# Kernel optimization log

Hardware: AMD Instinct MI355X
Metric: run time of the kernel (lower is better)

## Reference

```python
import jax, jax.numpy as jnp
import numpy as np

B, T, D = 32, 512, 256
F = 256  # duration_predictor_filter_size
K = 3    # kernel size, padding=1
MEL_MAX = 2304
EPS = 1e-5


def _conv1d(x, w, b):
    # x: [B, T, C_in], w: [C_out, C_in, K], 'same'-ish padding=1
    y = jax.lax.conv_general_dilated(
        x.transpose(0, 2, 1), w, window_strides=(1,), padding=[(1, 1)],
        dimension_numbers=("NCH", "OIH", "NCH"))
    return y.transpose(0, 2, 1) + b


def _layernorm(x, g, b):
    mu = jnp.mean(x, axis=-1, keepdims=True)
    var = jnp.mean(jnp.square(x - mu), axis=-1, keepdims=True)
    return (x - mu) * jax.lax.rsqrt(var + EPS) * g + b


def setup_inputs() -> dict:
    key = jax.random.key(0)
    ks = jax.random.split(key, 8)
    x = jax.random.normal(ks[0], (B, T, D), dtype=jnp.float32)
    target = jax.random.randint(ks[1], (B, T), 0, 8, dtype=jnp.int32)
    s = 0.02
    return {
        "x": x,
        "target": target,
        "mel_max_length": MEL_MAX,
        "conv1_w": jax.random.normal(ks[2], (F, D, K), dtype=jnp.float32) * s,
        "conv1_b": jnp.zeros((F,), jnp.float32),
        "ln1_g": jnp.ones((F,), jnp.float32),
        "ln1_b": jnp.zeros((F,), jnp.float32),
        "conv2_w": jax.random.normal(ks[3], (F, F, K), dtype=jnp.float32) * s,
        "conv2_b": jnp.zeros((F,), jnp.float32),
        "ln2_g": jnp.ones((F,), jnp.float32),
        "ln2_b": jnp.zeros((F,), jnp.float32),
        "lin_w": jax.random.normal(ks[4], (1, F), dtype=jnp.float32) * s,
        "lin_b": jnp.zeros((1,), jnp.float32),
    }


def reference(x, target, mel_max_length, conv1_w, conv1_b, ln1_g, ln1_b,
              conv2_w, conv2_b, ln2_g, ln2_b, lin_w, lin_b):
    # Variance_adaptor (duration predictor), eval-mode dropout = identity
    h = jax.nn.relu(_layernorm(_conv1d(x, conv1_w, conv1_b), ln1_g, ln1_b))
    h = jax.nn.relu(_layernorm(_conv1d(h, conv2_w, conv2_b), ln2_g, ln2_b))
    dur_pred = jax.nn.relu(jnp.einsum("btf,of->bto", h, lin_w) + lin_b)[..., 0]  # [B,T]

    # LR: alignment @ x, expressed as the equivalent duration-indexed gather.
    # alignment[b, t_out, j] = 1 iff cumsum(dur)[b,j-1] <= t_out < cumsum(dur)[b,j]
    cum = jnp.cumsum(target, axis=1)                    # [B, T]
    t_out = jnp.arange(mel_max_length, dtype=cum.dtype)  # [T_out]
    idx = jax.vmap(lambda c: jnp.searchsorted(c, t_out, side="right"))(cum)  # [B, T_out]
    valid = (t_out[None, :] < cum[:, -1:]).astype(x.dtype)                   # [B, T_out]
    gathered = jnp.take_along_axis(x, jnp.clip(idx, 0, T - 1)[:, :, None], axis=1)
    output = gathered * valid[:, :, None]                # zeros past total length (pad)
    return output, dur_pred
```

## Files before the change

kernel.cpp:

```cpp
#include <hip/hip_runtime.h>

typedef __attribute__((ext_vector_type(8))) short short8;
typedef __attribute__((ext_vector_type(4))) float floatx4;

typedef __attribute__((address_space(3))) unsigned int lds_u32;
typedef __attribute__((address_space(1))) const unsigned int glb_u32;

static __device__ __forceinline__ unsigned short f2bf(float f) {
    unsigned int u = __float_as_uint(f);
    return (unsigned short)((u + 0x7FFFu + ((u >> 16) & 1u)) >> 16);
}
static __device__ __forceinline__ void cp16(const ushort* g, ushort* l) {
    __builtin_amdgcn_global_load_lds((glb_u32*)g, (lds_u32*)l, 16, 0, 0);
}

__global__ __launch_bounds__(256)
void prep_kernel(const float* __restrict__ x, const float* __restrict__ w1,
                 const float* __restrict__ w2,
                 ushort* __restrict__ xb, ushort* __restrict__ h1b,
                 ushort* __restrict__ w1pb, ushort* __restrict__ w2pb)
{
    const int blk = blockIdx.x, tid = threadIdx.x;
    if (blk < 4112) {
        const int r = blk * 4 + (tid >> 6);
        const int c = (tid & 63) * 4;
        const int b = r / 514, tp = r % 514;
        ushort4 o;
        if (tp >= 1 && tp <= 512) {
            float4 v = *(const float4*)(x + ((size_t)(b * 512 + tp - 1) * 256 + c));
            o.x = f2bf(v.x); o.y = f2bf(v.y); o.z = f2bf(v.z); o.w = f2bf(v.w);
        } else {
            o.x = o.y = o.z = o.w = 0;
            *(ushort4*)(h1b + (size_t)r * 256 + c) = o;
        }
        *(ushort4*)(xb + (size_t)r * 256 + c) = o;
    } else {
        const bool second = blk >= 4880;
        const int e = (blk - (second ? 4880 : 4112)) * 256 + tid;
        const float* w = second ? w2 : w1;
        ushort* wpb = second ? w2pb : w1pb;
        const int f = e / 768, j = e % 768;
        const int c = j & 255, kr = j >> 8;
        const int s = j >> 6, kk = j & 63;
        wpb[s * 16384 + f * 64 + (((kk >> 3) ^ (f & 7)) << 3) + (kk & 7)]
            = f2bf(w[f * 768 + c * 3 + kr]);
    }
}

template<bool IS_CONV2>
__global__ __launch_bounds__(256, 2)
void conv_mfma_kernel(const ushort* __restrict__ xb,
                      const ushort* __restrict__ wpb,
                      const float* __restrict__ cbias,
                      const float* __restrict__ gamma, const float* __restrict__ beta,
                      const float* __restrict__ lw, const float* __restrict__ lb,
                      ushort* __restrict__ outb,
                      float* __restrict__ durp,
                      const float* __restrict__ x,
                      const int* __restrict__ target,
                      float* __restrict__ out0)
{
    __shared__ ushort As[32 * 64];
    __shared__ ushort Bs[256 * 64];
    __shared__ float sum_s[4][32], sq_s[4][32], mu_s[32], rs_s[32];
    __shared__ int cum[512], ps[256], sidx[64];

    const int tid = threadIdx.x;

    if (IS_CONV2 && blockIdx.x >= 512) {
        const int bg = blockIdx.x - 512;
        const int b = bg / 36, t0o = (bg % 36) * 64;
        const int v0 = target[b * 512 + 2 * tid];
        const int v1 = target[b * 512 + 2 * tid + 1];
        ps[tid] = v0 + v1;
        __syncthreads();
        for (int off = 1; off < 256; off <<= 1) {
            int t = (tid >= off) ? ps[tid - off] : 0;
            __syncthreads();
            ps[tid] += t;
            __syncthreads();
        }
        const int excl = tid ? ps[tid - 1] : 0;
        cum[2 * tid]     = excl + v0;
        cum[2 * tid + 1] = excl + v0 + v1;
        __syncthreads();
        const int total = cum[511];
        if (tid < 64) {
            int t = t0o + tid;
            int lo = 0, hi = 512;
            while (lo < hi) {
                int mid = (lo + hi) >> 1;
                if (cum[mid] <= t) lo = mid + 1; else hi = mid;
            }
            sidx[tid] = (t < total) ? ((lo < 512) ? lo : 511) : -1;
        }
        __syncthreads();
        const float4* x4 = (const float4*)x;
        float4* o4 = (float4*)out0;
        const int lane6 = tid & 63, g4 = tid >> 6;
        #pragma unroll 4
        for (int rr = 0; rr < 16; ++rr) {
            int r = rr * 4 + g4;
            int idx = sidx[r];
            float4 v = make_float4(0.f, 0.f, 0.f, 0.f);
            if (idx >= 0) v = x4[((size_t)(b * 512 + idx)) * 64 + lane6];
            o4[((size_t)(b * 2304 + t0o + r)) * 64 + lane6] = v;
        }
        return;
    }

    const int w_ = tid >> 6, lane = tid & 63;
    const int q = lane >> 4, col = lane & 15;
    const int b  = blockIdx.x & 31;
    const int t0 = (blockIdx.x >> 5) << 5;
    const int rot = blockIdx.x % 12;

    floatx4 acc[2][4] = {};
    const ushort* xbb = xb + (size_t)b * 514 * 256;
    const int arow = tid >> 3, aquad = (tid & 7) ^ (arow & 7);
    ushort* AsW = As + (size_t)w_ * 512;
    ushort* BsW = Bs + (size_t)w_ * 512;

    for (int s = 0; s < 12; ++s) {
        int se = s + rot; if (se >= 12) se -= 12;
        const int krow = se >> 2, cbo = (se & 3) << 6;
        cp16(xbb + (size_t)(t0 + krow + arow) * 256 + cbo + aquad * 8, AsW);
        const ushort* wsrc = wpb + (size_t)se * 16384 + w_ * 512 + lane * 8;
        #pragma unroll
        for (int i = 0; i < 8; ++i) cp16(wsrc + i * 2048, BsW + i * 2048);
        __syncthreads();
        short8 af[2][2], bf[4][2];
        #pragma unroll
        for (int mi = 0; mi < 2; ++mi)
            #pragma unroll
            for (int kh = 0; kh < 2; ++kh)
                af[mi][kh] = *(const short8*)((const char*)As
                    + (mi * 16 + col) * 128 + (((kh * 4 + q) ^ (col & 7)) * 16));
        #pragma unroll
        for (int ni = 0; ni < 4; ++ni)
            #pragma unroll
            for (int kh = 0; kh < 2; ++kh)
                bf[ni][kh] = *(const short8*)((const char*)Bs
                    + (w_ * 64 + ni * 16 + col) * 128 + (((kh * 4 + q) ^ (col & 7)) * 16));
        #pragma unroll
        for (int kh = 0; kh < 2; ++kh)
            #pragma unroll
            for (int mi = 0; mi < 2; ++mi)
                #pragma unroll
                for (int ni = 0; ni < 4; ++ni)
                    acc[mi][ni] = __builtin_amdgcn_mfma_f32_16x16x32_bf16(
                        af[mi][kh], bf[ni][kh], acc[mi][ni], 0, 0, 0);
        __syncthreads();
    }

    const int base_c = w_ * 64;
    float cb4[4], gm4[4], bt4[4];
    #pragma unroll
    for (int ni = 0; ni < 4; ++ni) {
        cb4[ni] = cbias[base_c + ni * 16 + col];
        gm4[ni] = gamma[base_c + ni * 16 + col];
        bt4[ni] = beta [base_c + ni * 16 + col];
    }
    float rsum[2][4] = {}, rsq[2][4] = {};
    #pragma unroll
    for (int mi = 0; mi < 2; ++mi)
        #pragma unroll
        for (int ni = 0; ni < 4; ++ni)
            #pragma unroll
            for (int r = 0; r < 4; ++r) {
                float v = acc[mi][ni][r] + cb4[ni];
                acc[mi][ni][r] = v;
                rsum[mi][r] += v;
                rsq [mi][r] += v * v;
            }
    #pragma unroll
    for (int mi = 0; mi < 2; ++mi)
        #pragma unroll
        for (int r = 0; r < 4; ++r) {
            float s = rsum[mi][r], ss = rsq[mi][r];
            #pragma unroll
            for (int d = 8; d > 0; d >>= 1) {
                s  += __shfl_down(s,  d, 16);
                ss += __shfl_down(ss, d, 16);
            }
            if (col == 0) {
                sum_s[w_][mi * 16 + q * 4 + r] = s;
                sq_s [w_][mi * 16 + q * 4 + r] = ss;
            }
        }
    __syncthreads();
    if (tid < 32) {
        float s  = sum_s[0][tid] + sum_s[1][tid] + sum_s[2][tid] + sum_s[3][tid];
        float ss = sq_s [0][tid] + sq_s [1][tid] + sq_s [2][tid] + sq_s [3][tid];
        float mu = s * (1.f / 256.f);
        mu_s[tid] = mu;
        rs_s[tid] = rsqrtf(ss * (1.f / 256.f) - mu * mu + 1e-5f);
    }
    __syncthreads();

    if (!IS_CONV2) {
        #pragma unroll
        for (int mi = 0; mi < 2; ++mi)
            #pragma unroll
            for (int ni = 0; ni < 4; ++ni)
                #pragma unroll
                for (int r = 0; r < 4; ++r) {
                    int row = mi * 16 + q * 4 + r;
                    float v = (acc[mi][ni][r] - mu_s[row]) * rs_s[row] * gm4[ni] + bt4[ni];
                    outb[((size_t)b * 514 + t0 + row + 1) * 256 + base_c + ni * 16 + col]
                        = f2bf(fmaxf(v, 0.f));
                }
    } else {
        float lw4[4];
        #pragma unroll
        for (int ni = 0; ni < 4; ++ni) lw4[ni] = lw[base_c + ni * 16 + col];
        float dsum[2][4] = {};
        #pragma unroll
        for (int mi = 0; mi < 2; ++mi)
            #pragma unroll
            for (int ni = 0; ni < 4; ++ni)
                #pragma unroll
                for (int r = 0; r < 4; ++r) {
                    int row = mi * 16 + q * 4 + r;
                    float v = (acc[mi][ni][r] - mu_s[row]) * rs_s[row] * gm4[ni] + bt4[ni];
                    dsum[mi][r] += fmaxf(v, 0.f) * lw4[ni];
                }
        #pragma unroll
        for (int mi = 0; mi < 2; ++mi)
            #pragma unroll
            for (int r = 0; r < 4; ++r) {
                float s = dsum[mi][r];
                #pragma unroll
                for (int d = 8; d > 0; d >>= 1) s += __shfl_down(s, d, 16);
                if (col == 0) sum_s[w_][mi * 16 + q * 4 + r] = s;
            }
        __syncthreads();
        if (tid < 32)
            durp[b * 512 + t0 + tid] = fmaxf(sum_s[0][tid] + sum_s[1][tid]
                                           + sum_s[2][tid] + sum_s[3][tid] + lb[0], 0.f);
    }
}

extern "C" void kernel_launch(void* const* d_in, const int* in_sizes, int n_in,
                              void* d_out, int out_size, void* d_ws, size_t ws_size,
                              hipStream_t stream) {
    const float* x      = (const float*)d_in[0];
    const int*   target = (const int*)  d_in[1];
    const float* c1w = (const float*)d_in[3];
    const float* c1b = (const float*)d_in[4];
    const float* g1  = (const float*)d_in[5];
    const float* b1  = (const float*)d_in[6];
    const float* c2w = (const float*)d_in[7];
    const float* c2b = (const float*)d_in[8];
    const float* g2  = (const float*)d_in[9];
    const float* b2  = (const float*)d_in[10];
    const float* lw  = (const float*)d_in[11];
    const float* lb  = (const float*)d_in[12];

    const size_t PADEL = (size_t)32 * 514 * 256;
    ushort* xb   = (ushort*)d_ws;
    ushort* h1b  = xb + PADEL;
    ushort* w1pb = h1b + PADEL;
    ushort* w2pb = w1pb + 196608;

    float* out0 = (float*)d_out;
    float* durp = out0 + (size_t)32 * 2304 * 256;

    prep_kernel<<<5648, 256, 0, stream>>>(x, c1w, c2w, xb, h1b, w1pb, w2pb);
    conv_mfma_kernel<false><<<512, 256, 0, stream>>>(
        xb, w1pb, c1b, g1, b1, nullptr, nullptr, h1b, nullptr,
        nullptr, nullptr, nullptr);
    conv_mfma_kernel<true><<<512 + 1152, 256, 0, stream>>>(
        h1b, w2pb, c2b, g2, b2, lw, lb, nullptr, durp,
        x, target, out0);
}
```

Baseline: 146.6 us.

## Double-buffer conv MFMA loads with 512-thread blocks and 64-row tiles

Conv blocks grow to 512 threads covering 64 time rows, so each weight stage is shared across twice as many rows, halving global weight traffic per output. The K loop becomes double-buffered, loading step s+1 into LDS while step s runs its MFMAs, with explicit vmcnt waits and raw barriers. Conv1 output is staged through LDS and written with coalesced 16-byte stores, and the gather blocks now handle 128 output rows each with a single 512-wide scan. The trade-off is fewer blocks in the grid (256 conv blocks), larger LDS use per block, and removal of the per-block K rotation that spread weight reads.

New measurement: 153.3 us. 1.05x slower.

```diff
diff --git a/kernel.cpp b/kernel.cpp
--- a/kernel.cpp
+++ b/kernel.cpp
@@ -48,7 +48,7 @@
 }
 
 template<bool IS_CONV2>
-__global__ __launch_bounds__(256, 2)
+__global__ __launch_bounds__(512, 2)
 void conv_mfma_kernel(const ushort* __restrict__ xb,
                       const ushort* __restrict__ wpb,
                       const float* __restrict__ cbias,
@@ -60,33 +60,26 @@
                       const int* __restrict__ target,
                       float* __restrict__ out0)
 {
-    __shared__ ushort As[32 * 64];
-    __shared__ ushort Bs[256 * 64];
-    __shared__ float sum_s[4][32], sq_s[4][32], mu_s[32], rs_s[32];
-    __shared__ int cum[512], ps[256], sidx[64];
+    __shared__ ushort stage[2][20480];
+    __shared__ float sum_s[4][64], sq_s[4][64], mu_s[64], rs_s[64];
+    __shared__ int cum[512], sidx[128];
 
     const int tid = threadIdx.x;
 
-    if (IS_CONV2 && blockIdx.x >= 512) {
-        const int bg = blockIdx.x - 512;
-        const int b = bg / 36, t0o = (bg % 36) * 64;
-        const int v0 = target[b * 512 + 2 * tid];
-        const int v1 = target[b * 512 + 2 * tid + 1];
-        ps[tid] = v0 + v1;
+    if (IS_CONV2 && blockIdx.x >= 256) {
+        const int g = blockIdx.x - 256;
+        const int b = g / 18, seg = g % 18;
+        cum[tid] = target[b * 512 + tid];
         __syncthreads();
-        for (int off = 1; off < 256; off <<= 1) {
-            int t = (tid >= off) ? ps[tid - off] : 0;
+        for (int off = 1; off < 512; off <<= 1) {
+            int v = (tid >= off) ? cum[tid - off] : 0;
             __syncthreads();
-            ps[tid] += t;
+            cum[tid] += v;
             __syncthreads();
         }
-        const int excl = tid ? ps[tid - 1] : 0;
-        cum[2 * tid]     = excl + v0;
-        cum[2 * tid + 1] = excl + v0 + v1;
-        __syncthreads();
         const int total = cum[511];
-        if (tid < 64) {
-            int t = t0o + tid;
+        if (tid < 128) {
+            int t = seg * 128 + tid;
             int lo = 0, hi = 512;
             while (lo < hi) {
                 int mid = (lo + hi) >> 1;
@@ -97,51 +90,73 @@
         __syncthreads();
         const float4* x4 = (const float4*)x;
         float4* o4 = (float4*)out0;
-        const int lane6 = tid & 63, g4 = tid >> 6;
+        const int lane6 = tid & 63, g8 = tid >> 6;
         #pragma unroll 4
-        for (int rr = 0; rr < 16; ++rr) {
-            int r = rr * 4 + g4;
+        for (int it = 0; it < 16; ++it) {
+            int r = it * 8 + g8;
             int idx = sidx[r];
             float4 v = make_float4(0.f, 0.f, 0.f, 0.f);
             if (idx >= 0) v = x4[((size_t)(b * 512 + idx)) * 64 + lane6];
-            o4[((size_t)(b * 2304 + t0o + r)) * 64 + lane6] = v;
+            o4[((size_t)(b * 2304 + seg * 128 + r)) * 64 + lane6] = v;
         }
         return;
     }
 
     const int w_ = tid >> 6, lane = tid & 63;
     const int q = lane >> 4, col = lane & 15;
-    const int b  = blockIdx.x & 31;
-    const int t0 = (blockIdx.x >> 5) << 5;
-    const int rot = blockIdx.x % 12;
+    const int rg = w_ >> 2, colw = w_ & 3;
+    const int b  = blockIdx.x >> 3;
+    const int t0 = (blockIdx.x & 7) << 6;
+
+    const ushort* inb = xb + (size_t)b * 514 * 256;
+    const int arow = tid >> 3;
+    const int ajs  = (tid & 7) ^ (arow & 7);
 
     floatx4 acc[2][4] = {};
-    const ushort* xbb = xb + (size_t)b * 514 * 256;
-    const int arow = tid >> 3, aquad = (tid & 7) ^ (arow & 7);
-    ushort* AsW = As + (size_t)w_ * 512;
-    ushort* BsW = Bs + (size_t)w_ * 512;
+
+#define STAGE_STEP(S, BUF)                                                       \
+    {                                                                            \
+        const int krow = (S) >> 2, cb = ((S) & 3) << 6;                          \
+        cp16(inb + (size_t)(t0 + krow + arow) * 256 + cb + ajs * 8,              \
+             (BUF) + w_ * 512);                                                  \
+        const ushort* wsrc = wpb + (size_t)(S) * 16384;                          \
+        _Pragma("unroll")                                                        \
+        for (int i = 0; i < 4; ++i)                                              \
+            cp16(wsrc + (i * 512 + tid) * 8,                                     \
+                 (BUF) + 4096 + i * 4096 + w_ * 512);                            \
+    }
+
+    STAGE_STEP(0, stage[0])
 
     for (int s = 0; s < 12; ++s) {
-        int se = s + rot; if (se >= 12) se -= 12;
-        const int krow = se >> 2, cbo = (se & 3) << 6;
-        cp16(xbb + (size_t)(t0 + krow + arow) * 256 + cbo + aquad * 8, AsW);
-        const ushort* wsrc = wpb + (size_t)se * 16384 + w_ * 512 + lane * 8;
-        #pragma unroll
-        for (int i = 0; i < 8; ++i) cp16(wsrc + i * 2048, BsW + i * 2048);
-        __syncthreads();
+        __builtin_amdgcn_s_barrier();
+        if (s < 11) {
+            STAGE_STEP(s + 1, stage[(s + 1) & 1])
+            asm volatile("s_waitcnt vmcnt(5)" ::: "memory");
+        } else {
+            asm volatile("s_waitcnt vmcnt(0)" ::: "memory");
+        }
+        __builtin_amdgcn_s_barrier();
+
+        const ushort* At = stage[s & 1];
+        const ushort* Bt = stage[s & 1] + 4096;
         short8 af[2][2], bf[4][2];
         #pragma unroll
-        for (int mi = 0; mi < 2; ++mi)
+        for (int mi = 0; mi < 2; ++mi) {
+            const int ri = rg * 32 + mi * 16 + col;
             #pragma unroll
             for (int kh = 0; kh < 2; ++kh)
-                af[mi][kh] = *(const short8*)((const char*)As
-                    + (mi * 16 + col) * 128 + (((kh * 4 + q) ^ (col & 7)) * 16));
-        #pragma unroll
-        for (int ni = 0; ni < 4; ++ni)
+                af[mi][kh] = *(const short8*)((const char*)At
+                    + ri * 128 + (((kh * 4 + q) ^ (ri & 7)) * 16));
+        }
+        #pragma unroll
+        for (int ni = 0; ni < 4; ++ni) {
+            const int n = colw * 64 + ni * 16 + col;
             #pragma unroll
             for (int kh = 0; kh < 2; ++kh)
-                bf[ni][kh] = *(const short8*)((const char*)Bs
-                    + (w_ * 64 + ni * 16 + col) * 128 + (((kh * 4 + q) ^ (col & 7)) * 16));
+                bf[ni][kh] = *(const short8*)((const char*)Bt
+                    + n * 128 + (((kh * 4 + q) ^ (n & 7)) * 16));
+        }
         #pragma unroll
         for (int kh = 0; kh < 2; ++kh)
             #pragma unroll
@@ -150,16 +165,16 @@
                 for (int ni = 0; ni < 4; ++ni)
                     acc[mi][ni] = __builtin_amdgcn_mfma_f32_16x16x32_bf16(
                         af[mi][kh], bf[ni][kh], acc[mi][ni], 0, 0, 0);
-        __syncthreads();
-    }
-
-    const int base_c = w_ * 64;
+    }
+#undef STAGE_STEP
+
+    const int bc0 = colw * 64;
     float cb4[4], gm4[4], bt4[4];
     #pragma unroll
     for (int ni = 0; ni < 4; ++ni) {
-        cb4[ni] = cbias[base_c + ni * 16 + col];
-        gm4[ni] = gamma[base_c + ni * 16 + col];
-        bt4[ni] = beta [base_c + ni * 16 + col];
+        cb4[ni] = cbias[bc0 + ni * 16 + col];
+        gm4[ni] = gamma[bc0 + ni * 16 + col];
+        bt4[ni] = beta [bc0 + ni * 16 + col];
     }
     float rsum[2][4] = {}, rsq[2][4] = {};
     #pragma unroll
@@ -184,12 +199,13 @@
                 ss += __shfl_down(ss, d, 16);
             }
             if (col == 0) {
-                sum_s[w_][mi * 16 + q * 4 + r] = s;
-                sq_s [w_][mi * 16 + q * 4 + r] = ss;
+                const int row = rg * 32 + mi * 16 + q * 4 + r;
+                sum_s[colw][row] = s;
+                sq_s [colw][row] = ss;
             }
         }
     __syncthreads();
-    if (tid < 32) {
+    if (tid < 64) {
         float s  = sum_s[0][tid] + sum_s[1][tid] + sum_s[2][tid] + sum_s[3][tid];
         float ss = sq_s [0][tid] + sq_s [1][tid] + sq_s [2][tid] + sq_s [3][tid];
         float mu = s * (1.f / 256.f);
@@ -199,21 +215,29 @@
     __syncthreads();
 
     if (!IS_CONV2) {
+        ushort* yb = stage[0];
         #pragma unroll
         for (int mi = 0; mi < 2; ++mi)
             #pragma unroll
             for (int ni = 0; ni < 4; ++ni)
                 #pragma unroll
                 for (int r = 0; r < 4; ++r) {
-                    int row = mi * 16 + q * 4 + r;
+                    const int row = rg * 32 + mi * 16 + q * 4 + r;
                     float v = (acc[mi][ni][r] - mu_s[row]) * rs_s[row] * gm4[ni] + bt4[ni];
-                    outb[((size_t)b * 514 + t0 + row + 1) * 256 + base_c + ni * 16 + col]
-                        = f2bf(fmaxf(v, 0.f));
+                    yb[row * 256 + bc0 + ni * 16 + col] = f2bf(fmaxf(v, 0.f));
                 }
+        __syncthreads();
+        #pragma unroll
+        for (int i = 0; i < 4; ++i) {
+            const int idx = i * 512 + tid;
+            const int row = idx >> 5, c = idx & 31;
+            *(short8*)(outb + ((size_t)b * 514 + t0 + row + 1) * 256 + c * 8)
+                = *(const short8*)(yb + row * 256 + c * 8);
+        }
     } else {
         float lw4[4];
         #pragma unroll
-        for (int ni = 0; ni < 4; ++ni) lw4[ni] = lw[base_c + ni * 16 + col];
+        for (int ni = 0; ni < 4; ++ni) lw4[ni] = lw[bc0 + ni * 16 + col];
         float dsum[2][4] = {};
         #pragma unroll
         for (int mi = 0; mi < 2; ++mi)
@@ -221,7 +245,7 @@
             for (int ni = 0; ni < 4; ++ni)
                 #pragma unroll
                 for (int r = 0; r < 4; ++r) {
-                    int row = mi * 16 + q * 4 + r;
+                    const int row = rg * 32 + mi * 16 + q * 4 + r;
                     float v = (acc[mi][ni][r] - mu_s[row]) * rs_s[row] * gm4[ni] + bt4[ni];
                     dsum[mi][r] += fmaxf(v, 0.f) * lw4[ni];
                 }
@@ -232,10 +256,10 @@
                 float s = dsum[mi][r];
                 #pragma unroll
                 for (int d = 8; d > 0; d >>= 1) s += __shfl_down(s, d, 16);
-                if (col == 0) sum_s[w_][mi * 16 + q * 4 + r] = s;
+                if (col == 0) sum_s[colw][rg * 32 + mi * 16 + q * 4 + r] = s;
             }
         __syncthreads();
-        if (tid < 32)
+        if (tid < 64)
             durp[b * 512 + t0 + tid] = fmaxf(sum_s[0][tid] + sum_s[1][tid]
                                            + sum_s[2][tid] + sum_s[3][tid] + lb[0], 0.f);
     }
@@ -267,10 +291,10 @@
     float* durp = out0 + (size_t)32 * 2304 * 256;
 
     prep_kernel<<<5648, 256, 0, stream>>>(x, c1w, c2w, xb, h1b, w1pb, w2pb);
-    conv_mfma_kernel<false><<<512, 256, 0, stream>>>(
+    conv_mfma_kernel<false><<<256, 512, 0, stream>>>(
         xb, w1pb, c1b, g1, b1, nullptr, nullptr, h1b, nullptr,
         nullptr, nullptr, nullptr);
-    conv_mfma_kernel<true><<<512 + 1152, 256, 0, stream>>>(
+    conv_mfma_kernel<true><<<256 + 576, 512, 0, stream>>>(
         h1b, w2pb, c2b, g2, b2, lw, lb, nullptr, durp,
         x, target, out0);
 }
```
